# Performance work log

Measured on AMD Instinct MI355X. Metric: run time of the kernel, lower is better.

## Reference

```python
import jax, jax.numpy as jnp
import numpy as np

K = 3  # kernel size
PAD = K // 2


def setup_inputs() -> dict:
    key = jax.random.key(0)
    k1, k2, k3 = jax.random.split(key, 3)
    B, C, H, W = 8, 192, 128, 128
    x = jax.random.normal(k1, (B, C, H, W), dtype=jnp.float32)
    kernel = 0.02 * jax.random.normal(k2, (C, K * K), dtype=jnp.float32)
    gate_w = 0.02 * jax.random.normal(k3, (C,), dtype=jnp.float32)
    gate_b = jnp.zeros((C,), dtype=jnp.float32)
    return {"x": x, "kernel": kernel, "gate_w": gate_w, "gate_b": gate_b}


def reference(x, kernel, gate_w, gate_b):
    B, C, H, W = x.shape
    # F.unfold with zero padding: patches[b,c,ki*K+kj,h,w] = x_pad[b,c,h+ki,w+kj]
    xp = jnp.pad(x, ((0, 0), (0, 0), (PAD, PAD), (PAD, PAD)))
    patches = jnp.stack(
        [xp[:, :, i:i + H, j:j + W] for i in range(K) for j in range(K)],
        axis=2,
    )  # [B, C, K*K, H, W]
    # depthwise 1x1 gate: per-channel scale + bias, then sigmoid
    theta = jax.nn.sigmoid(x * gate_w[None, :, None, None] + gate_b[None, :, None, None])
    # max-plus: max_v [ f(u-v) + theta(u) * k(v) ]
    scored = patches + theta[:, :, None] * kernel[None, :, :, None, None]
    return jnp.max(scored, axis=2)  # [B, C, H, W]
```

## Files before the change

kernel.cpp:

```cpp
#include <hip/hip_runtime.h>
#include <math.h>

#define BB 8
#define CC 192
#define HH 128
#define WW 128
#define RPS 16
#define DPF 6
#define NB  (DPF + 1)

typedef float vf4 __attribute__((ext_vector_type(4)));

__device__ __forceinline__ float col9(float a0, float a1, float a2,
                                      float b0, float b1, float b2,
                                      float c0, float c1, float c2,
                                      float th, const float* kk) {
    float m;
    m = fmaf(th, kk[0], a0);
    m = fmaxf(m, fmaf(th, kk[1], a1));
    m = fmaxf(m, fmaf(th, kk[2], a2));
    m = fmaxf(m, fmaf(th, kk[3], b0));
    m = fmaxf(m, fmaf(th, kk[4], b1));
    m = fmaxf(m, fmaf(th, kk[5], b2));
    m = fmaxf(m, fmaf(th, kk[6], c0));
    m = fmaxf(m, fmaf(th, kk[7], c1));
    m = fmaxf(m, fmaf(th, kk[8], c2));
    return m;
}

__global__ __launch_bounds__(256) void dynmorph_kernel(
    const float* __restrict__ x,
    const float* __restrict__ kern,
    const float* __restrict__ gw,
    const float* __restrict__ gb,
    float* __restrict__ out)
{
    const int tid  = threadIdx.x;
    const int lane = tid & 63;
    const int wg   = lane & 31;
    const int rs   = (tid >> 6) * 2 + (lane >> 5);
    const int col  = wg * 4;
    const int r0   = rs * RPS;

    const int bc = blockIdx.x;
    const int c  = bc % CC;

    const float* xp = x   + (size_t)bc * (HH * WW);
    float*       op = out + (size_t)bc * (HH * WW);

    float kk[9];
#pragma unroll
    for (int i = 0; i < 9; ++i) kk[i] = kern[c * 9 + i];
    const float gwc = gw[c];
    const float gbc = gb[c];

    auto ld = [&](int i) -> vf4 {
        const int g = r0 - 1 + i;
        if (g >= 0 && g < HH) return *(const vf4*)(xp + g * WW + col);
        return (vf4)(0.0f);
    };

    vf4   buf[NB];
    float lfh[RPS + 2], rth[RPS + 2];

#pragma unroll
    for (int i = 0; i < DPF; ++i) buf[i % NB] = ld(i);
    __builtin_amdgcn_sched_barrier(0);

#pragma unroll
    for (int i = 0; i < 2; ++i) {
        const vf4 t = buf[i % NB];
        const float l = __shfl_up(t.w, 1);
        const float r = __shfl_down(t.x, 1);
        lfh[i] = (wg == 0)  ? 0.0f : l;
        rth[i] = (wg == 31) ? 0.0f : r;
    }

#pragma unroll
    for (int g = 0; g < RPS; ++g) {
        if (g + DPF < RPS + 2) {
            buf[(g + DPF) % NB] = ld(g + DPF);
        }
        __builtin_amdgcn_sched_barrier(0);

        {
            const vf4 t = buf[(g + 2) % NB];
            const float l = __shfl_up(t.w, 1);
            const float r = __shfl_down(t.x, 1);
            lfh[g + 2] = (wg == 0)  ? 0.0f : l;
            rth[g + 2] = (wg == 31) ? 0.0f : r;
        }

        const vf4 A  = buf[g % NB];
        const vf4 B  = buf[(g + 1) % NB];
        const vf4 Cv = buf[(g + 2) % NB];

        const float t0 = __builtin_amdgcn_rcpf(1.0f + __expf(-fmaf(B.x, gwc, gbc)));
        const float t1 = __builtin_amdgcn_rcpf(1.0f + __expf(-fmaf(B.y, gwc, gbc)));
        const float t2 = __builtin_amdgcn_rcpf(1.0f + __expf(-fmaf(B.z, gwc, gbc)));
        const float t3 = __builtin_amdgcn_rcpf(1.0f + __expf(-fmaf(B.w, gwc, gbc)));

        vf4 o;
        o.x = col9(lfh[g],   A.x, A.y,
                   lfh[g+1], B.x, B.y,
                   lfh[g+2], Cv.x, Cv.y, t0, kk);
        o.y = col9(A.x, A.y, A.z,
                   B.x, B.y, B.z,
                   Cv.x, Cv.y, Cv.z, t1, kk);
        o.z = col9(A.y, A.z, A.w,
                   B.y, B.z, B.w,
                   Cv.y, Cv.z, Cv.w, t2, kk);
        o.w = col9(A.z, A.w, rth[g],
                   B.z, B.w, rth[g+1],
                   Cv.z, Cv.w, rth[g+2], t3, kk);

        *(vf4*)(op + (r0 + g) * WW + col) = o;
    }
}

extern "C" void kernel_launch(void* const* d_in, const int* in_sizes, int n_in,
                              void* d_out, int out_size, void* d_ws, size_t ws_size,
                              hipStream_t stream) {
    const float* x    = (const float*)d_in[0];
    const float* kern = (const float*)d_in[1];
    const float* gw   = (const float*)d_in[2];
    const float* gb   = (const float*)d_in[3];
    float* out        = (float*)d_out;

    dim3 grid(BB * CC);
    dim3 block(256);
    dynmorph_kernel<<<grid, block, 0, stream>>>(x, kern, gw, gb, out);
}
```

Before: 183.5 us.

## Stage input rows through an LDS ring buffer instead of per-thread register stripes

Each workgroup now cycles 8-row groups through a 4-slot padded LDS ring. Rows are interleaved across threads (row = 8*g + rs) rather than each thread owning a contiguous 16-row stripe. Stencil neighbors are read from LDS with zero-padded halo columns, which removes the cross-lane shuffles and the duplicated halo-row global loads per stripe. The cost is two workgroup barriers per step and LDS traffic, and global prefetch depth is cut to about two groups.

```diff
diff --git a/kernel.cpp b/kernel.cpp
--- a/kernel.cpp
+++ b/kernel.cpp
@@ -5,11 +5,15 @@
 #define CC 192
 #define HH 128
 #define WW 128
-#define RPS 16
-#define DPF 6
-#define NB  (DPF + 1)
+
+#define GR    8
+#define NG    16
+#define ROWF  136
+#define SLOTF (GR * ROWF)
+#define LDSF  (4 * SLOTF)
 
 typedef float vf4 __attribute__((ext_vector_type(4)));
+typedef float vf2 __attribute__((ext_vector_type(2)));
 
 __device__ __forceinline__ float col9(float a0, float a1, float a2,
                                       float b0, float b1, float b2,
@@ -35,12 +39,13 @@
     const float* __restrict__ gb,
     float* __restrict__ out)
 {
+    __shared__ float smem[LDSF];
+
     const int tid  = threadIdx.x;
     const int lane = tid & 63;
     const int wg   = lane & 31;
     const int rs   = (tid >> 6) * 2 + (lane >> 5);
     const int col  = wg * 4;
-    const int r0   = rs * RPS;
 
     const int bc = blockIdx.x;
     const int c  = bc % CC;
@@ -54,67 +59,80 @@
     const float gwc = gw[c];
     const float gbc = gb[c];
 
-    auto ld = [&](int i) -> vf4 {
-        const int g = r0 - 1 + i;
-        if (g >= 0 && g < HH) return *(const vf4*)(xp + g * WW + col);
+    {
+        const int row = tid >> 3, p = tid & 7;
+        smem[row * ROWF + (p < 4 ? p : 128 + p)] = 0.0f;
+    }
+
+    auto ldgrp = [&](int q) -> vf4 {
+        const int r = GR * q - GR + rs;
+        if (r >= 0 && r < HH) return *(const vf4*)(xp + r * WW + col);
         return (vf4)(0.0f);
     };
+    auto wrgrp = [&](int q, vf4 v) {
+        *(vf4*)(&smem[(q & 3) * SLOTF + rs * ROWF + 4 + col]) = v;
+    };
 
-    vf4   buf[NB];
-    float lfh[RPS + 2], rth[RPS + 2];
+    {
+        vf4 t0 = ldgrp(0), t1 = ldgrp(1), t2 = ldgrp(2);
+        wrgrp(0, t0); wrgrp(1, t1); wrgrp(2, t2);
+    }
+    vf4 buf[3];
+    buf[0] = ldgrp(3);
+    buf[1] = ldgrp(4);
+    buf[2] = (vf4)(0.0f);
+    asm volatile("s_waitcnt lgkmcnt(0)" ::: "memory");
+    __builtin_amdgcn_s_barrier();
 
 #pragma unroll
-    for (int i = 0; i < DPF; ++i) buf[i % NB] = ld(i);
-    __builtin_amdgcn_sched_barrier(0);
+    for (int g = 0; g < NG; ++g) {
+        if (g + 3 <= 17) wrgrp(g + 3, buf[g % 3]);
+        if (g + 5 <= 17) buf[(g + 2) % 3] = ldgrp(g + 5);
+        __builtin_amdgcn_sched_barrier(0);
+        asm volatile("s_waitcnt lgkmcnt(0)" ::: "memory");
+        __builtin_amdgcn_s_barrier();
 
-#pragma unroll
-    for (int i = 0; i < 2; ++i) {
-        const vf4 t = buf[i % NB];
-        const float l = __shfl_up(t.w, 1);
-        const float r = __shfl_down(t.x, 1);
-        lfh[i] = (wg == 0)  ? 0.0f : l;
-        rth[i] = (wg == 31) ? 0.0f : r;
-    }
+        const int ro  = GR * g + rs;
+        const int prm = ro + 7;
+        const int pr0 = ro + 8;
+        const int prp = ro + 9;
+        const float* bm = &smem[((prm >> 3) & 3) * SLOTF + (prm & 7) * ROWF + 4];
+        const float* b0 = &smem[((pr0 >> 3) & 3) * SLOTF + (pr0 & 7) * ROWF + 4];
+        const float* bp = &smem[((prp >> 3) & 3) * SLOTF + (prp & 7) * ROWF + 4];
 
-#pragma unroll
-    for (int g = 0; g < RPS; ++g) {
-        if (g + DPF < RPS + 2) {
-            buf[(g + DPF) % NB] = ld(g + DPF);
-        }
-        __builtin_amdgcn_sched_barrier(0);
+        const vf2 Lm = *(const vf2*)(bm + col - 2);
+        const vf4 Mm = *(const vf4*)(bm + col);
+        const vf2 Rm = *(const vf2*)(bm + col + 4);
+        const vf2 L0 = *(const vf2*)(b0 + col - 2);
+        const vf4 M0 = *(const vf4*)(b0 + col);
+        const vf2 R0 = *(const vf2*)(b0 + col + 4);
+        const vf2 Lp = *(const vf2*)(bp + col - 2);
+        const vf4 Mp = *(const vf4*)(bp + col);
+        const vf2 Rp = *(const vf2*)(bp + col + 4);
 
-        {
-            const vf4 t = buf[(g + 2) % NB];
-            const float l = __shfl_up(t.w, 1);
-            const float r = __shfl_down(t.x, 1);
-            lfh[g + 2] = (wg == 0)  ? 0.0f : l;
-            rth[g + 2] = (wg == 31) ? 0.0f : r;
-        }
-
-        const vf4 A  = buf[g % NB];
-        const vf4 B  = buf[(g + 1) % NB];
-        const vf4 Cv = buf[(g + 2) % NB];
-
-        const float t0 = __builtin_amdgcn_rcpf(1.0f + __expf(-fmaf(B.x, gwc, gbc)));
-        const float t1 = __builtin_amdgcn_rcpf(1.0f + __expf(-fmaf(B.y, gwc, gbc)));
-        const float t2 = __builtin_amdgcn_rcpf(1.0f + __expf(-fmaf(B.z, gwc, gbc)));
-        const float t3 = __builtin_amdgcn_rcpf(1.0f + __expf(-fmaf(B.w, gwc, gbc)));
+        const float t0 = __builtin_amdgcn_rcpf(1.0f + __expf(-fmaf(M0.x, gwc, gbc)));
+        const float t1 = __builtin_amdgcn_rcpf(1.0f + __expf(-fmaf(M0.y, gwc, gbc)));
+        const float t2 = __builtin_amdgcn_rcpf(1.0f + __expf(-fmaf(M0.z, gwc, gbc)));
+        const float t3 = __builtin_amdgcn_rcpf(1.0f + __expf(-fmaf(M0.w, gwc, gbc)));
 
         vf4 o;
-        o.x = col9(lfh[g],   A.x, A.y,
-                   lfh[g+1], B.x, B.y,
-                   lfh[g+2], Cv.x, Cv.y, t0, kk);
-        o.y = col9(A.x, A.y, A.z,
-                   B.x, B.y, B.z,
-                   Cv.x, Cv.y, Cv.z, t1, kk);
-        o.z = col9(A.y, A.z, A.w,
-                   B.y, B.z, B.w,
-                   Cv.y, Cv.z, Cv.w, t2, kk);
-        o.w = col9(A.z, A.w, rth[g],
-                   B.z, B.w, rth[g+1],
-                   Cv.z, Cv.w, rth[g+2], t3, kk);
+        o.x = col9(Lm.y, Mm.x, Mm.y,
+                   L0.y, M0.x, M0.y,
+                   Lp.y, Mp.x, Mp.y, t0, kk);
+        o.y = col9(Mm.x, Mm.y, Mm.z,
+                   M0.x, M0.y, M0.z,
+                   Mp.x, Mp.y, Mp.z, t1, kk);
+        o.z = col9(Mm.y, Mm.z, Mm.w,
+                   M0.y, M0.z, M0.w,
+                   Mp.y, Mp.z, Mp.w, t2, kk);
+        o.w = col9(Mm.z, Mm.w, Rm.x,
+                   M0.z, M0.w, R0.x,
+                   Mp.z, Mp.w, Rp.x, t3, kk);
 
-        *(vf4*)(op + (r0 + g) * WW + col) = o;
+        *(vf4*)(op + ro * WW + col) = o;
+
+        __builtin_amdgcn_sched_barrier(0);
+        __builtin_amdgcn_s_barrier();
     }
 }
 
```

Result: no change. 185.0 us (+0.8%).

## Redistribute work as 4-row strips per half-wave over a persistent-style wave grid

Applied to the files above, without the earlier changes.

Instead of one block per (batch, channel) image with each half-wave streaming 16 rows through a rotating prefetch buffer, each wave now processes four independent tasks in sequence. In each task a half-wave loads 6 rows up front and computes 4 output rows. The intent is to raise memory-level parallelism by issuing all loads at once and spreading tiles across the whole GPU in a strided order. In exchange the halo overhead goes up (6 loads per 4 rows instead of 18 per 16), and per-channel parameters are reloaded for every task. The grid must be sized to NWAVE/4 blocks, but the launch code is not shown as changed (still BB*CC = 1536 blocks, which matches 6144/4).

```diff
diff --git a/kernel.cpp b/kernel.cpp
--- a/kernel.cpp
+++ b/kernel.cpp
@@ -5,9 +5,9 @@
 #define CC 192
 #define HH 128
 #define WW 128
-#define RPS 16
-#define DPF 6
-#define NB  (DPF + 1)
+#define IMGF (HH * WW)
+#define NWAVE 6144
+#define NSTEP 4
 
 typedef float vf4 __attribute__((ext_vector_type(4)));
 
@@ -38,83 +38,71 @@
     const int tid  = threadIdx.x;
     const int lane = tid & 63;
     const int wg   = lane & 31;
-    const int rs   = (tid >> 6) * 2 + (lane >> 5);
+    const int hf   = lane >> 5;
     const int col  = wg * 4;
-    const int r0   = rs * RPS;
-
-    const int bc = blockIdx.x;
-    const int c  = bc % CC;
-
-    const float* xp = x   + (size_t)bc * (HH * WW);
-    float*       op = out + (size_t)bc * (HH * WW);
-
-    float kk[9];
-#pragma unroll
-    for (int i = 0; i < 9; ++i) kk[i] = kern[c * 9 + i];
-    const float gwc = gw[c];
-    const float gbc = gb[c];
-
-    auto ld = [&](int i) -> vf4 {
-        const int g = r0 - 1 + i;
-        if (g >= 0 && g < HH) return *(const vf4*)(xp + g * WW + col);
-        return (vf4)(0.0f);
-    };
-
-    vf4   buf[NB];
-    float lfh[RPS + 2], rth[RPS + 2];
+    const int wv   = __builtin_amdgcn_readfirstlane((int)(threadIdx.x >> 6));
+    const int w    = blockIdx.x * 4 + wv;
 
 #pragma unroll
-    for (int i = 0; i < DPF; ++i) buf[i % NB] = ld(i);
-    __builtin_amdgcn_sched_barrier(0);
+    for (int s = 0; s < NSTEP; ++s) {
+        const int p   = s * NWAVE + w;
+        const int bc  = p >> 4;
+        const int c   = bc % CC;
+        const int ir0 = ((p & 15) << 3) + (hf << 2);
+
+        const float* xb = x   + (size_t)bc * IMGF;
+        float*       ob = out + (size_t)bc * IMGF;
+
+        float kk[9];
+#pragma unroll
+        for (int i = 0; i < 9; ++i) kk[i] = kern[c * 9 + i];
+        const float gwc = gw[c];
+        const float gbc = gb[c];
+
+        vf4 buf[6];
+#pragma unroll
+        for (int j = 0; j < 6; ++j) {
+            const int lr = ir0 - 1 + j;
+            buf[j] = (lr >= 0 && lr < HH) ? *(const vf4*)(xb + lr * WW + col)
+                                          : (vf4)(0.0f);
+        }
+
+        float lf[6], rt[6];
+#pragma unroll
+        for (int j = 0; j < 6; ++j) {
+            const float l = __shfl_up(buf[j].w, 1);
+            const float r = __shfl_down(buf[j].x, 1);
+            lf[j] = (wg == 0)  ? 0.0f : l;
+            rt[j] = (wg == 31) ? 0.0f : r;
+        }
 
 #pragma unroll
-    for (int i = 0; i < 2; ++i) {
-        const vf4 t = buf[i % NB];
-        const float l = __shfl_up(t.w, 1);
-        const float r = __shfl_down(t.x, 1);
-        lfh[i] = (wg == 0)  ? 0.0f : l;
-        rth[i] = (wg == 31) ? 0.0f : r;
-    }
+        for (int j = 0; j < 4; ++j) {
+            const vf4 A  = buf[j];
+            const vf4 B  = buf[j + 1];
+            const vf4 Cv = buf[j + 2];
 
-#pragma unroll
-    for (int g = 0; g < RPS; ++g) {
-        if (g + DPF < RPS + 2) {
-            buf[(g + DPF) % NB] = ld(g + DPF);
+            const float t0 = __builtin_amdgcn_rcpf(1.0f + __expf(-fmaf(B.x, gwc, gbc)));
+            const float t1 = __builtin_amdgcn_rcpf(1.0f + __expf(-fmaf(B.y, gwc, gbc)));
+            const float t2 = __builtin_amdgcn_rcpf(1.0f + __expf(-fmaf(B.z, gwc, gbc)));
+            const float t3 = __builtin_amdgcn_rcpf(1.0f + __expf(-fmaf(B.w, gwc, gbc)));
+
+            vf4 o;
+            o.x = col9(lf[j],     A.x, A.y,
+                       lf[j + 1], B.x, B.y,
+                       lf[j + 2], Cv.x, Cv.y, t0, kk);
+            o.y = col9(A.x, A.y, A.z,
+                       B.x, B.y, B.z,
+                       Cv.x, Cv.y, Cv.z, t1, kk);
+            o.z = col9(A.y, A.z, A.w,
+                       B.y, B.z, B.w,
+                       Cv.y, Cv.z, Cv.w, t2, kk);
+            o.w = col9(A.z, A.w, rt[j],
+                       B.z, B.w, rt[j + 1],
+                       Cv.z, Cv.w, rt[j + 2], t3, kk);
+
+            *(vf4*)(ob + (ir0 + j) * WW + col) = o;
         }
-        __builtin_amdgcn_sched_barrier(0);
-
-        {
-            const vf4 t = buf[(g + 2) % NB];
-            const float l = __shfl_up(t.w, 1);
-            const float r = __shfl_down(t.x, 1);
-            lfh[g + 2] = (wg == 0)  ? 0.0f : l;
-            rth[g + 2] = (wg == 31) ? 0.0f : r;
-        }
-
-        const vf4 A  = buf[g % NB];
-        const vf4 B  = buf[(g + 1) % NB];
-        const vf4 Cv = buf[(g + 2) % NB];
-
-        const float t0 = __builtin_amdgcn_rcpf(1.0f + __expf(-fmaf(B.x, gwc, gbc)));
-        const float t1 = __builtin_amdgcn_rcpf(1.0f + __expf(-fmaf(B.y, gwc, gbc)));
-        const float t2 = __builtin_amdgcn_rcpf(1.0f + __expf(-fmaf(B.z, gwc, gbc)));
-        const float t3 = __builtin_amdgcn_rcpf(1.0f + __expf(-fmaf(B.w, gwc, gbc)));
-
-        vf4 o;
-        o.x = col9(lfh[g],   A.x, A.y,
-                   lfh[g+1], B.x, B.y,
-                   lfh[g+2], Cv.x, Cv.y, t0, kk);
-        o.y = col9(A.x, A.y, A.z,
-                   B.x, B.y, B.z,
-                   Cv.x, Cv.y, Cv.z, t1, kk);
-        o.z = col9(A.y, A.z, A.w,
-                   B.y, B.z, B.w,
-                   Cv.y, Cv.z, Cv.w, t2, kk);
-        o.w = col9(A.z, A.w, rth[g],
-                   B.z, B.w, rth[g+1],
-                   Cv.z, Cv.w, rth[g+2], t3, kk);
-
-        *(vf4*)(op + (r0 + g) * WW + col) = o;
     }
 }
 
```

After: 181.5 us. About the same (-1.1%).
